# Kernel optimization log

Measured on AMD Instinct MI355X. Metric: run time of the kernel, lower is better.

## Reference

```python
import jax, jax.numpy as jnp
import numpy as np

B, T, N = 32, 64, 36
VD, H, S = 2048, 512, 300


def setup_inputs() -> dict:
    key = jax.random.key(0)
    ks = jax.random.split(key, 24)
    sc = 0.02
    d = {
        "visual": jax.random.normal(ks[0], (B, T, VD), jnp.float32),
        "objects": jax.random.normal(ks[1], (B, N, H), jnp.float32),
        # linear_layer
        "lin_W": jax.random.normal(ks[2], (H, VD), jnp.float32) * sc,
        "lin_b": jnp.zeros((H,), jnp.float32),
        # W, U projections
        "W_W": jax.random.normal(ks[3], (H, H), jnp.float32) * sc,
        "W_b": jnp.zeros((H,), jnp.float32),
        "U_W": jax.random.normal(ks[4], (H, H), jnp.float32) * sc,
        "U_b": jnp.zeros((H,), jnp.float32),
        # additive attention bias (torch.ones init)
        "b_attn": jnp.ones((H,), jnp.float32),
        # scoring vector w: Linear(H, 1)
        "w_W": jax.random.normal(ks[5], (1, H), jnp.float32) * sc,
        "w_b": jnp.zeros((1,), jnp.float32),
        # BiLSTM: input 2H, hidden H//2 per direction; gate order i,f,g,o
        "Wih_f": jax.random.normal(ks[6], (4 * (H // 2), 2 * H), jnp.float32) * sc,
        "Whh_f": jax.random.normal(ks[7], (4 * (H // 2), H // 2), jnp.float32) * sc,
        "bih_f": jnp.zeros((4 * (H // 2),), jnp.float32),
        "bhh_f": jnp.zeros((4 * (H // 2),), jnp.float32),
        "Wih_b": jax.random.normal(ks[8], (4 * (H // 2), 2 * H), jnp.float32) * sc,
        "Whh_b": jax.random.normal(ks[9], (4 * (H // 2), H // 2), jnp.float32) * sc,
        "bih_b": jnp.zeros((4 * (H // 2),), jnp.float32),
        "bhh_b": jnp.zeros((4 * (H // 2),), jnp.float32),
        # fc_layer
        "fc_W": jax.random.normal(ks[10], (S, H), jnp.float32) * sc,
        "fc_b": jnp.zeros((S,), jnp.float32),
    }
    return d


def _lstm(x, Wih, Whh, b):
    """Unidirectional LSTM over time. x: [B, T, D] -> [B, T, Hc]."""
    bsz = x.shape[0]
    Hc = Whh.shape[1]

    def step(carry, xt):
        h, c = carry
        g = xt @ Wih.T + h @ Whh.T + b          # [B, 4Hc]
        i, f, gg, o = jnp.split(g, 4, axis=-1)  # torch gate order i,f,g,o
        c = jax.nn.sigmoid(f) * c + jax.nn.sigmoid(i) * jnp.tanh(gg)
        h = jax.nn.sigmoid(o) * jnp.tanh(c)
        return (h, c), h

    h0 = jnp.zeros((bsz, Hc), x.dtype)
    _, hs = jax.lax.scan(step, (h0, h0), jnp.swapaxes(x, 0, 1))
    return jnp.swapaxes(hs, 0, 1)


def reference(visual, objects, lin_W, lin_b, W_W, W_b, U_W, U_b, b_attn,
              w_W, w_b, Wih_f, Whh_f, bih_f, bhh_f, Wih_b, Whh_b, bih_b,
              bhh_b, fc_W, fc_b):
    f3d = visual @ lin_W.T + lin_b                 # [B, T, H]
    Wf = f3d @ W_W.T + W_b                         # [B, T, H]
    Uo = objects @ U_W.T + U_b                     # [B, N, H]
    # broadcast additive attention: [B, T, N, H]
    attn_feat = Wf[:, :, None, :] + Uo[:, None, :, :] + b_attn
    scores = jnp.tanh(attn_feat) @ w_W.T + w_b     # [B, T, N, 1]
    attn_w = jax.nn.softmax(scores, axis=-2)       # softmax over objects N
    attn_obj = (attn_w * attn_feat).sum(axis=-2)   # [B, T, H]
    feats = jnp.concatenate([f3d, attn_obj], axis=-1)  # [B, T, 2H]
    out_f = _lstm(feats, Wih_f, Whh_f, bih_f + bhh_f)
    out_b = _lstm(feats[:, ::-1, :], Wih_b, Whh_b, bih_b + bhh_b)[:, ::-1, :]
    output = jnp.concatenate([out_f, out_b], axis=-1)  # [B, T, H]
    action = jnp.max(output, axis=1)                   # [B, H]
    action_semantics = action @ fc_W.T + fc_b          # [B, S]
    return output, action_semantics
```

## Files before the change

kernel.cpp:

```cpp
#include <hip/hip_runtime.h>
#include <hip/hip_bf16.h>
#include <type_traits>


typedef __hip_bfloat16 bf16;
typedef unsigned int uint32;
typedef __attribute__((ext_vector_type(8))) short s8v;
typedef __attribute__((ext_vector_type(4))) float f4v;
typedef __attribute__((ext_vector_type(4))) int   i32x4;

__device__ inline f4v mfma16(s8v a, s8v b, f4v c) {
    return __builtin_amdgcn_mfma_f32_16x16x32_bf16(a, b, c, 0, 0, 0);
}
__device__ inline float sigf(float x) {
    return __builtin_amdgcn_rcpf(1.f + __expf(-x));
}
__device__ inline float tanh_(float x) {
    return 1.f - 2.f * __builtin_amdgcn_rcpf(1.f + __expf(2.f * x));
}
__device__ inline void gload_lds16(const bf16* g, bf16* l) {
    __builtin_amdgcn_global_load_lds(
        (const __attribute__((address_space(1))) void*)g,
        (__attribute__((address_space(3))) void*)l, 16, 0, 0);
}

struct CvtJobs {
    const float* src[9];
    bf16*        dst[9];
    int          start[10];
};

__global__ __launch_bounds__(256) void cvt_kernel(CvtJobs jobs) {
    int blk = blockIdx.x;
    int j = 0;
#pragma unroll
    for (int i = 1; i < 9; ++i) if (blk >= jobs.start[i]) j = i;
    int off = (blk - jobs.start[j]) * 1024 + threadIdx.x * 4;
    float4 v = *(const float4*)(jobs.src[j] + off);
    union { bf16 h[4]; uint2 u; } p;
    p.h[0] = __float2bfloat16(v.x);
    p.h[1] = __float2bfloat16(v.y);
    p.h[2] = __float2bfloat16(v.z);
    p.h[3] = __float2bfloat16(v.w);
    *(uint2*)(jobs.dst[j] + off) = p.u;
}

template <typename CT>
__global__ __launch_bounds__(256) void gemm_tile(
    const bf16* __restrict__ A, int lda,
    const bf16* __restrict__ W,
    const float* __restrict__ b1, const float* __restrict__ b2,
    CT* __restrict__ C, int ldc,
    int K, int tiles_n, int permuteTB)
{
    __shared__ bf16 As[128 * 64];
    __shared__ bf16 Bs[128 * 64];

    int tid = threadIdx.x;
    int w = tid >> 6, lane = tid & 63;
    int lo = lane & 15, hi = lane >> 4;
    int mt = blockIdx.x / tiles_n, nt = blockIdx.x % tiles_n;
    int wm = w >> 1, wn = w & 1;

    const bf16* Ab = A + (size_t)(mt * 128) * lda;
    const bf16* Wb = W + (size_t)(nt * 128) * K;

    f4v acc[4][4];
#pragma unroll
    for (int m = 0; m < 4; ++m)
#pragma unroll
        for (int n = 0; n < 4; ++n) acc[m][n] = (f4v){0.f, 0.f, 0.f, 0.f};

    int wbase = tid & 192;

    for (int k0 = 0; k0 < K; k0 += 64) {
#pragma unroll
        for (int i = 0; i < 4; ++i) {
            int ci = i * 256 + tid;
            int row = ci >> 3, c = ci & 7;
            int gc = c ^ (row & 7);
            gload_lds16(Ab + (size_t)row * lda + k0 + gc * 8,
                        As + (i * 256 + wbase) * 8);
            gload_lds16(Wb + (size_t)row * K + k0 + gc * 8,
                        Bs + (i * 256 + wbase) * 8);
        }
        __syncthreads();

#pragma unroll
        for (int kt = 0; kt < 2; ++kt) {
            s8v a[4], b[4];
            int sw = ((kt * 4 + hi) ^ (lo & 7)) * 8;
#pragma unroll
            for (int m = 0; m < 4; ++m)
                a[m] = *(const s8v*)(As + (wm * 64 + m * 16 + lo) * 64 + sw);
#pragma unroll
            for (int n = 0; n < 4; ++n)
                b[n] = *(const s8v*)(Bs + (wn * 64 + n * 16 + lo) * 64 + sw);
#pragma unroll
            for (int m = 0; m < 4; ++m)
#pragma unroll
                for (int n = 0; n < 4; ++n)
                    acc[m][n] = mfma16(a[m], b[n], acc[m][n]);
        }
        __syncthreads();
    }

#pragma unroll
    for (int n = 0; n < 4; ++n) {
        int cc = nt * 128 + wn * 64 + n * 16 + lo;
        float bv = (b1 ? b1[cc] : 0.f) + (b2 ? b2[cc] : 0.f);
#pragma unroll
        for (int m = 0; m < 4; ++m) {
            int rbase = mt * 128 + wm * 64 + m * 16 + hi * 4;
#pragma unroll
            for (int i = 0; i < 4; ++i) {
                int r = rbase + i;
                int rr = permuteTB ? ((r & 63) * 32 + (r >> 6)) : r;
                float v = acc[m][n][i] + bv;
                if constexpr (std::is_same<CT, float>::value)
                    C[(size_t)rr * ldc + cc] = v;
                else
                    C[(size_t)rr * ldc + cc] = __float2bfloat16(v);
            }
        }
    }
}

__global__ __launch_bounds__(256) void attn_kernel(
    const float* __restrict__ Wf,
    const float* __restrict__ Uo,
    const float* __restrict__ wW,
    const float* __restrict__ wB,
    bf16* __restrict__ feats)
{
    int bt = blockIdx.x, b = bt >> 6;
    int wv = threadIdx.x >> 6, lane = threadIdx.x & 63;
    __shared__ float s_aw[36];

    float wfr[8], wr[8];
    const float* wfrow = Wf + (size_t)bt * 512 + lane * 8;
#pragma unroll
    for (int i = 0; i < 8; ++i) {
        wfr[i] = wfrow[i];
        wr[i]  = wW[lane * 8 + i];
    }
    float wbv = wB[0];

    for (int n = wv; n < 36; n += 4) {
        const float* uo = Uo + ((size_t)b * 36 + n) * 512 + lane * 8;
        float s = 0.f;
#pragma unroll
        for (int i = 0; i < 8; ++i) s += wr[i] * tanh_(wfr[i] + uo[i]);
#pragma unroll
        for (int off = 32; off; off >>= 1) s += __shfl_xor(s, off);
        if (lane == 0) s_aw[n] = s + wbv;
    }
    __syncthreads();
    if (threadIdx.x == 0) {
        float mx = -1e30f;
#pragma unroll
        for (int n = 0; n < 36; ++n) mx = fmaxf(mx, s_aw[n]);
        float e[36], sum = 0.f;
#pragma unroll
        for (int n = 0; n < 36; ++n) { e[n] = __expf(s_aw[n] - mx); sum += e[n]; }
        float r = __builtin_amdgcn_rcpf(sum);
#pragma unroll
        for (int n = 0; n < 36; ++n) s_aw[n] = e[n] * r;
    }
    __syncthreads();

    int h0 = threadIdx.x * 2;
    const float* wf2 = Wf + (size_t)bt * 512 + h0;
    float a0 = wf2[0], a1 = wf2[1];
    for (int n = 0; n < 36; ++n) {
        float awn = s_aw[n];
        const float* uo = Uo + ((size_t)b * 36 + n) * 512 + h0;
        a0 += awn * uo[0];
        a1 += awn * uo[1];
    }
    feats[(size_t)bt * 1024 + 512 + h0]     = __float2bfloat16(a0);
    feats[(size_t)bt * 1024 + 512 + h0 + 1] = __float2bfloat16(a1);
}

__device__ inline void poll4(const int* p, int need) {
    for (;;) {
        i32x4 f;
        asm volatile("global_load_dwordx4 %0, %1, off sc1\n\t"
                     "s_waitcnt vmcnt(0)"
                     : "=v"(f) : "v"(p) : "memory");
        if (f[0] >= need && f[1] >= need && f[2] >= need && f[3] >= need)
            break;
    }
}

__device__ inline void load_h16(const uint32* pF, const uint32* pB, s8v* aF) {
    asm volatile(
        "global_load_dwordx4 %0, %16, off sc1\n\t"
        "global_load_dwordx4 %1, %16, off offset:64 sc1\n\t"
        "global_load_dwordx4 %2, %16, off offset:128 sc1\n\t"
        "global_load_dwordx4 %3, %16, off offset:192 sc1\n\t"
        "global_load_dwordx4 %4, %16, off offset:256 sc1\n\t"
        "global_load_dwordx4 %5, %16, off offset:320 sc1\n\t"
        "global_load_dwordx4 %6, %16, off offset:384 sc1\n\t"
        "global_load_dwordx4 %7, %16, off offset:448 sc1\n\t"
        "global_load_dwordx4 %8, %17, off sc1\n\t"
        "global_load_dwordx4 %9, %17, off offset:64 sc1\n\t"
        "global_load_dwordx4 %10, %17, off offset:128 sc1\n\t"
        "global_load_dwordx4 %11, %17, off offset:192 sc1\n\t"
        "global_load_dwordx4 %12, %17, off offset:256 sc1\n\t"
        "global_load_dwordx4 %13, %17, off offset:320 sc1\n\t"
        "global_load_dwordx4 %14, %17, off offset:384 sc1\n\t"
        "global_load_dwordx4 %15, %17, off offset:448 sc1\n\t"
        "s_waitcnt vmcnt(0)"
        : "=v"(aF[0]), "=v"(aF[1]), "=v"(aF[2]), "=v"(aF[3]),
          "=v"(aF[4]), "=v"(aF[5]), "=v"(aF[6]), "=v"(aF[7]),
          "=v"(aF[8]), "=v"(aF[9]), "=v"(aF[10]), "=v"(aF[11]),
          "=v"(aF[12]), "=v"(aF[13]), "=v"(aF[14]), "=v"(aF[15])
        : "v"(pF), "v"(pB)
        : "memory");
}

__global__ __launch_bounds__(256, 1) void lstm_kernel(
    const bf16* __restrict__ WhhF, const bf16* __restrict__ WhhB,
    const float* __restrict__ gatesF, const float* __restrict__ gatesB,
    uint32* __restrict__ hx,
    float* __restrict__ out,
    int* __restrict__ bar)
{
    int bi  = blockIdx.x;
    int g   = bi >> 2;
    int pid = bi & 3;
    int jb  = pid * 64;
    int wv = threadIdx.x >> 6, lane = threadIdx.x & 63;
    int lo = lane & 15, hi = lane >> 4;
    int j0 = jb + wv * 16;

    uint32* hxg  = hx + (size_t)g * 8192;
    int*    flags = bar + g * 16;

    s8v whh[2][4][8];
#pragma unroll
    for (int q = 0; q < 4; ++q)
#pragma unroll
        for (int kt = 0; kt < 8; ++kt) {
            whh[0][q][kt] = *(const s8v*)(WhhF + (size_t)(q * 256 + j0 + lo) * 256 + kt * 32 + hi * 8);
            whh[1][q][kt] = *(const s8v*)(WhhB + (size_t)(q * 256 + j0 + lo) * 256 + kt * 32 + hi * 8);
        }

    int jbw = jb >> 1;
    for (int x = threadIdx.x; x < 1024; x += 256) {
        int d = x >> 9, b = (x >> 5) & 15, jw = jbw + (x & 31);
        __hip_atomic_store(&hxg[d * 4096 + b * 128 + jw], 0u,
                           __ATOMIC_RELAXED, __HIP_MEMORY_SCOPE_AGENT);
    }
    __syncthreads();
    if (threadIdx.x == 0)
        __hip_atomic_store(&flags[pid], 1, __ATOMIC_RELAXED,
                           __HIP_MEMORY_SCOPE_AGENT);

    poll4(flags, 1);
    s8v aF[16];
    {
        const uint32* pF = hxg + lo * 128 + hi * 4;
        load_h16(pF, pF + 4096, aF);
    }

    float cstf[4] = {0.f,0.f,0.f,0.f}, cstb[4] = {0.f,0.f,0.f,0.f};

    for (int t = 0; t < 64; ++t) {
        int tpF = t, tpB = 63 - t;
        int slot = (t + 1) & 1;

        float gvf[4][4], gvb[4][4];
#pragma unroll
        for (int i = 0; i < 4; ++i) {
            int bg = g * 16 + hi * 4 + i;
#pragma unroll
            for (int q = 0; q < 4; ++q) {
                gvf[q][i] = gatesF[(size_t)tpF * 32768 + bg * 1024 + q * 256 + j0 + lo];
                gvb[q][i] = gatesB[(size_t)tpB * 32768 + bg * 1024 + q * 256 + j0 + lo];
            }
        }

        float hvf[4];
        {
            f4v acc[4];
#pragma unroll
            for (int q = 0; q < 4; ++q) acc[q] = (f4v){0.f,0.f,0.f,0.f};
#pragma unroll
            for (int kt = 0; kt < 8; ++kt)
#pragma unroll
                for (int q = 0; q < 4; ++q)
                    acc[q] = mfma16(aF[kt], whh[0][q][kt], acc[q]);
#pragma unroll
            for (int i = 0; i < 4; ++i) {
                float xi = acc[0][i] + gvf[0][i];
                float xf = acc[1][i] + gvf[1][i];
                float xg = acc[2][i] + gvf[2][i];
                float xo = acc[3][i] + gvf[3][i];
                float c = sigf(xf) * cstf[i] + sigf(xi) * tanh_(xg);
                cstf[i] = c;
                hvf[i] = sigf(xo) * tanh_(c);
            }
        }
        if (t < 63) {
            uint32* hw = hxg + slot * 2048;
#pragma unroll
            for (int i = 0; i < 4; ++i) {
                float o2 = __shfl_xor(hvf[i], 1);
                if (!(lane & 1)) {
                    uint32 pk = (uint32)__bfloat16_as_ushort(__float2bfloat16(hvf[i]))
                              | ((uint32)__bfloat16_as_ushort(__float2bfloat16(o2)) << 16);
                    __hip_atomic_store(&hw[(hi * 4 + i) * 128 + ((j0 + lo) >> 1)], pk,
                                       __ATOMIC_RELAXED, __HIP_MEMORY_SCOPE_AGENT);
                }
            }
        }

        float hvb[4];
        {
            f4v acc[4];
#pragma unroll
            for (int q = 0; q < 4; ++q) acc[q] = (f4v){0.f,0.f,0.f,0.f};
#pragma unroll
            for (int kt = 0; kt < 8; ++kt)
#pragma unroll
                for (int q = 0; q < 4; ++q)
                    acc[q] = mfma16(aF[8 + kt], whh[1][q][kt], acc[q]);
#pragma unroll
            for (int i = 0; i < 4; ++i) {
                float xi = acc[0][i] + gvb[0][i];
                float xf = acc[1][i] + gvb[1][i];
                float xg = acc[2][i] + gvb[2][i];
                float xo = acc[3][i] + gvb[3][i];
                float c = sigf(xf) * cstb[i] + sigf(xi) * tanh_(xg);
                cstb[i] = c;
                hvb[i] = sigf(xo) * tanh_(c);
            }
        }
        if (t < 63) {
            uint32* hw = hxg + 4096 + slot * 2048;
#pragma unroll
            for (int i = 0; i < 4; ++i) {
                float o2 = __shfl_xor(hvb[i], 1);
                if (!(lane & 1)) {
                    uint32 pk = (uint32)__bfloat16_as_ushort(__float2bfloat16(hvb[i]))
                              | ((uint32)__bfloat16_as_ushort(__float2bfloat16(o2)) << 16);
                    __hip_atomic_store(&hw[(hi * 4 + i) * 128 + ((j0 + lo) >> 1)], pk,
                                       __ATOMIC_RELAXED, __HIP_MEMORY_SCOPE_AGENT);
                }
            }
        }

#pragma unroll
        for (int i = 0; i < 4; ++i) {
            int bg = g * 16 + hi * 4 + i;
            out[((size_t)bg * 64 + tpF) * 512 + j0 + lo]       = hvf[i];
            out[((size_t)bg * 64 + tpB) * 512 + 256 + j0 + lo] = hvb[i];
        }

        if (t < 63) {
            __syncthreads();
            if (threadIdx.x == 0)
                __hip_atomic_store(&flags[pid], t + 2, __ATOMIC_RELAXED,
                                   __HIP_MEMORY_SCOPE_AGENT);
            poll4(flags, t + 2);
            const uint32* pF = hxg + slot * 2048 + lo * 128 + hi * 4;
            load_h16(pF, pF + 4096, aF);
        }
    }
}

__global__ __launch_bounds__(256) void final_kernel(
    const float* __restrict__ out,
    const float* __restrict__ fcW,
    const float* __restrict__ fcb,
    float* __restrict__ osem)
{
    int b = blockIdx.x, tid = threadIdx.x;
    __shared__ float act[512];
    for (int h = tid; h < 512; h += 256) {
        float m = -1e30f;
        const float* p = out + (size_t)b * 64 * 512 + h;
#pragma unroll 8
        for (int t = 0; t < 64; ++t) m = fmaxf(m, p[t * 512]);
        act[h] = m;
    }
    __syncthreads();
    int wv = tid >> 6, lane = tid & 63;
    for (int s = wv; s < 300; s += 4) {
        const float* wrow = fcW + (size_t)s * 512 + lane * 8;
        float a = 0.f;
#pragma unroll
        for (int i = 0; i < 8; ++i) a += act[lane * 8 + i] * wrow[i];
#pragma unroll
        for (int off = 32; off; off >>= 1) a += __shfl_xor(a, off);
        if (lane == 0) osem[b * 300 + s] = a + fcb[s];
    }
}

extern "C" void kernel_launch(void* const* d_in, const int* in_sizes, int n_in,
                              void* d_out, int out_size, void* d_ws, size_t ws_size,
                              hipStream_t stream)
{
    const float* visual  = (const float*)d_in[0];
    const float* objects = (const float*)d_in[1];
    const float* lin_W   = (const float*)d_in[2];
    const float* lin_b   = (const float*)d_in[3];
    const float* W_W     = (const float*)d_in[4];
    const float* W_b     = (const float*)d_in[5];
    const float* U_W     = (const float*)d_in[6];
    const float* U_b     = (const float*)d_in[7];
    const float* b_attn  = (const float*)d_in[8];
    const float* w_W     = (const float*)d_in[9];
    const float* w_b     = (const float*)d_in[10];
    const float* Wih_f   = (const float*)d_in[11];
    const float* Whh_f   = (const float*)d_in[12];
    const float* bih_f   = (const float*)d_in[13];
    const float* bhh_f   = (const float*)d_in[14];
    const float* Wih_b   = (const float*)d_in[15];
    const float* Whh_b   = (const float*)d_in[16];
    const float* bih_b   = (const float*)d_in[17];
    const float* bhh_b   = (const float*)d_in[18];
    const float* fc_W    = (const float*)d_in[19];
    const float* fc_b    = (const float*)d_in[20];

    char* ws = (char*)d_ws;
    size_t o = 0;
    bf16*   feats   = (bf16*)(ws + o);   o += (size_t)2048 * 1024 * 2;
    float*  Wf      = (float*)(ws + o);  o += (size_t)2048 * 512 * 4;
    float*  Uo      = (float*)(ws + o);  o += (size_t)1152 * 512 * 4;
    float*  gatesF  = (float*)(ws + o);  o += (size_t)2048 * 1024 * 4;
    float*  gatesB  = (float*)(ws + o);  o += (size_t)2048 * 1024 * 4;
    uint32* hx      = (uint32*)(ws + o); o += (size_t)2 * 8192 * 4;
    int*    bar     = (int*)(ws + o);    o += 256;
    bf16*  visual_b  = (bf16*)(ws + o); o += (size_t)4194304 * 2;
    bf16*  objects_b = (bf16*)(ws + o); o += (size_t)589824 * 2;
    bf16*  lin_Wb    = (bf16*)(ws + o); o += (size_t)1048576 * 2;
    bf16*  W_Wb      = (bf16*)(ws + o); o += (size_t)262144 * 2;
    bf16*  U_Wb      = (bf16*)(ws + o); o += (size_t)262144 * 2;
    bf16*  Wih_fb    = (bf16*)(ws + o); o += (size_t)1048576 * 2;
    bf16*  Whh_fb    = (bf16*)(ws + o); o += (size_t)262144 * 2;
    bf16*  Wih_bb    = (bf16*)(ws + o); o += (size_t)1048576 * 2;
    bf16*  Whh_bb    = (bf16*)(ws + o); o += (size_t)262144 * 2;

    CvtJobs cj;
    const float* srcs[9] = {visual, objects, lin_W, W_W, U_W, Wih_f, Whh_f, Wih_b, Whh_b};
    bf16* dsts[9] = {visual_b, objects_b, lin_Wb, W_Wb, U_Wb, Wih_fb, Whh_fb, Wih_bb, Whh_bb};
    int ns[9] = {4194304, 589824, 1048576, 262144, 262144, 1048576, 262144, 1048576, 262144};
    int acc_b = 0;
    for (int i = 0; i < 9; ++i) {
        cj.src[i] = srcs[i];
        cj.dst[i] = dsts[i];
        cj.start[i] = acc_b;
        acc_b += ns[i] / 1024;
    }
    cj.start[9] = acc_b;

    dim3 blk(256);
    cvt_kernel<<<acc_b, blk, 0, stream>>>(cj);

    gemm_tile<bf16><<<64, blk, 0, stream>>>(visual_b, 2048, lin_Wb, lin_b, nullptr,
                                            feats, 1024, 2048, 4, 0);
    gemm_tile<float><<<36, blk, 0, stream>>>(objects_b, 512, U_Wb, U_b, b_attn,
                                             Uo, 512, 512, 4, 0);
    gemm_tile<float><<<64, blk, 0, stream>>>(feats, 1024, W_Wb, W_b, nullptr,
                                             Wf, 512, 512, 4, 0);
    attn_kernel<<<2048, blk, 0, stream>>>(Wf, Uo, w_W, w_b, feats);
    gemm_tile<float><<<128, blk, 0, stream>>>(feats, 1024, Wih_fb, bih_f, bhh_f,
                                              gatesF, 1024, 1024, 8, 1);
    gemm_tile<float><<<128, blk, 0, stream>>>(feats, 1024, Wih_bb, bih_b, bhh_b,
                                              gatesB, 1024, 1024, 8, 1);
    lstm_kernel<<<8, blk, 0, stream>>>(Whh_fb, Whh_bb, gatesF, gatesB, hx,
                                       (float*)d_out, bar);
    final_kernel<<<32, blk, 0, stream>>>((float*)d_out, fc_W, fc_b,
                                         (float*)d_out + 1048576);
}
```

Measured before the change: 591.7 us.

## Replace cross-block LSTM barrier with per-block recurrence; merge GEMM launches, bf16 gates

The LSTM recurrence is restructured so that each 512-thread block owns one direction and 16 batch rows with all 256 hidden units. The whole Whh matrix is held in registers plus LDS, and h is exchanged through shared memory with __syncthreads. This replaces the old global-memory flag polling across 4 blocks per group. The input-gate GEMMs are merged into a single launch that writes bf16 gates, and the pre-GEMMs are fused into one launch with smaller 64-row tiles for more blocks. Softmax in the attention kernel now uses wave shuffles instead of a single thread. The trade-off is that only 4 blocks run the serial recurrence, each doing more MFMA work per step, and storing gates in bf16 loses precision.

New measurement: 782.6 us. 1.32x slower.

```diff
diff --git a/kernel.cpp b/kernel.cpp
--- a/kernel.cpp
+++ b/kernel.cpp
@@ -5,9 +5,9 @@
 
 typedef __hip_bfloat16 bf16;
 typedef unsigned int uint32;
+typedef unsigned short ushort_t;
 typedef __attribute__((ext_vector_type(8))) short s8v;
 typedef __attribute__((ext_vector_type(4))) float f4v;
-typedef __attribute__((ext_vector_type(4))) int   i32x4;
 
 __device__ inline f4v mfma16(s8v a, s8v b, f4v c) {
     return __builtin_amdgcn_mfma_f32_16x16x32_bf16(a, b, c, 0, 0, 0);
@@ -17,6 +17,12 @@
 }
 __device__ inline float tanh_(float x) {
     return 1.f - 2.f * __builtin_amdgcn_rcpf(1.f + __expf(2.f * x));
+}
+__device__ inline float bf2f(ushort_t u) {
+    union { uint32 i; float f; } p; p.i = (uint32)u << 16; return p.f;
+}
+__device__ inline ushort_t f2bf(float f) {
+    return __bfloat16_as_ushort(__float2bfloat16(f));
 }
 __device__ inline void gload_lds16(const bf16* g, bf16* l) {
     __builtin_amdgcn_global_load_lds(
@@ -45,29 +51,25 @@
     *(uint2*)(jobs.dst[j] + off) = p.u;
 }
 
-template <typename CT>
-__global__ __launch_bounds__(256) void gemm_tile(
+template <int MT>
+__device__ inline void gemm_body(
+    bf16* As, bf16* Bs,
     const bf16* __restrict__ A, int lda,
     const bf16* __restrict__ W,
     const float* __restrict__ b1, const float* __restrict__ b2,
-    CT* __restrict__ C, int ldc,
-    int K, int tiles_n, int permuteTB)
-{
-    __shared__ bf16 As[128 * 64];
-    __shared__ bf16 Bs[128 * 64];
-
+    void* C, int ldc, int K, int mt, int nt, int obf, int permuteTB)
+{
     int tid = threadIdx.x;
     int w = tid >> 6, lane = tid & 63;
     int lo = lane & 15, hi = lane >> 4;
-    int mt = blockIdx.x / tiles_n, nt = blockIdx.x % tiles_n;
     int wm = w >> 1, wn = w & 1;
 
-    const bf16* Ab = A + (size_t)(mt * 128) * lda;
+    const bf16* Ab = A + (size_t)(mt * (MT * 32)) * lda;
     const bf16* Wb = W + (size_t)(nt * 128) * K;
 
-    f4v acc[4][4];
-#pragma unroll
-    for (int m = 0; m < 4; ++m)
+    f4v acc[MT][4];
+#pragma unroll
+    for (int m = 0; m < MT; ++m)
 #pragma unroll
         for (int n = 0; n < 4; ++n) acc[m][n] = (f4v){0.f, 0.f, 0.f, 0.f};
 
@@ -75,12 +77,18 @@
 
     for (int k0 = 0; k0 < K; k0 += 64) {
 #pragma unroll
-        for (int i = 0; i < 4; ++i) {
+        for (int i = 0; i < MT; ++i) {
             int ci = i * 256 + tid;
             int row = ci >> 3, c = ci & 7;
             int gc = c ^ (row & 7);
             gload_lds16(Ab + (size_t)row * lda + k0 + gc * 8,
                         As + (i * 256 + wbase) * 8);
+        }
+#pragma unroll
+        for (int i = 0; i < 4; ++i) {
+            int ci = i * 256 + tid;
+            int row = ci >> 3, c = ci & 7;
+            int gc = c ^ (row & 7);
             gload_lds16(Wb + (size_t)row * K + k0 + gc * 8,
                         Bs + (i * 256 + wbase) * 8);
         }
@@ -88,16 +96,16 @@
 
 #pragma unroll
         for (int kt = 0; kt < 2; ++kt) {
-            s8v a[4], b[4];
+            s8v a[MT], b[4];
             int sw = ((kt * 4 + hi) ^ (lo & 7)) * 8;
 #pragma unroll
-            for (int m = 0; m < 4; ++m)
-                a[m] = *(const s8v*)(As + (wm * 64 + m * 16 + lo) * 64 + sw);
+            for (int m = 0; m < MT; ++m)
+                a[m] = *(const s8v*)(As + (wm * (MT * 16) + m * 16 + lo) * 64 + sw);
 #pragma unroll
             for (int n = 0; n < 4; ++n)
                 b[n] = *(const s8v*)(Bs + (wn * 64 + n * 16 + lo) * 64 + sw);
 #pragma unroll
-            for (int m = 0; m < 4; ++m)
+            for (int m = 0; m < MT; ++m)
 #pragma unroll
                 for (int n = 0; n < 4; ++n)
                     acc[m][n] = mfma16(a[m], b[n], acc[m][n]);
@@ -110,20 +118,61 @@
         int cc = nt * 128 + wn * 64 + n * 16 + lo;
         float bv = (b1 ? b1[cc] : 0.f) + (b2 ? b2[cc] : 0.f);
 #pragma unroll
-        for (int m = 0; m < 4; ++m) {
-            int rbase = mt * 128 + wm * 64 + m * 16 + hi * 4;
+        for (int m = 0; m < MT; ++m) {
+            int rbase = mt * (MT * 32) + wm * (MT * 16) + m * 16 + hi * 4;
 #pragma unroll
             for (int i = 0; i < 4; ++i) {
                 int r = rbase + i;
                 int rr = permuteTB ? ((r & 63) * 32 + (r >> 6)) : r;
                 float v = acc[m][n][i] + bv;
-                if constexpr (std::is_same<CT, float>::value)
-                    C[(size_t)rr * ldc + cc] = v;
-                else
-                    C[(size_t)rr * ldc + cc] = __float2bfloat16(v);
+                if (obf) ((bf16*)C)[(size_t)rr * ldc + cc] = __float2bfloat16(v);
+                else     ((float*)C)[(size_t)rr * ldc + cc] = v;
             }
         }
     }
+}
+
+__global__ __launch_bounds__(256) void gemm_pre(
+    const bf16* visual_b, const bf16* lin_Wb, const float* lin_b,
+    const bf16* objects_b, const bf16* U_Wb, const float* U_b,
+    const float* b_attn, bf16* feats, float* Uo)
+{
+    __shared__ bf16 As[64 * 64];
+    __shared__ bf16 Bs[128 * 64];
+    int blk = blockIdx.x;
+    if (blk < 128)
+        gemm_body<2>(As, Bs, visual_b, 2048, lin_Wb, lin_b, nullptr,
+                     feats, 1024, 2048, blk / 4, blk % 4, 1, 0);
+    else {
+        int bi = blk - 128;
+        gemm_body<2>(As, Bs, objects_b, 512, U_Wb, U_b, b_attn,
+                     Uo, 512, 512, bi / 4, bi % 4, 0, 0);
+    }
+}
+
+__global__ __launch_bounds__(256) void gemm_wf(
+    const bf16* feats, const bf16* W_Wb, const float* W_b, float* Wf)
+{
+    __shared__ bf16 As[64 * 64];
+    __shared__ bf16 Bs[128 * 64];
+    gemm_body<2>(As, Bs, feats, 1024, W_Wb, W_b, nullptr,
+                 Wf, 512, 512, blockIdx.x / 4, blockIdx.x % 4, 0, 0);
+}
+
+__global__ __launch_bounds__(256) void gemm_gates(
+    const bf16* feats, const bf16* Wih_fb, const bf16* Wih_bb,
+    const float* bih_f, const float* bhh_f,
+    const float* bih_b, const float* bhh_b, bf16* gatesFB)
+{
+    __shared__ bf16 As[128 * 64];
+    __shared__ bf16 Bs[128 * 64];
+    int sel = blockIdx.x >> 7;
+    int blk = blockIdx.x & 127;
+    gemm_body<4>(As, Bs, feats, 1024,
+                 sel ? Wih_bb : Wih_fb,
+                 sel ? bih_b : bih_f, sel ? bhh_b : bhh_f,
+                 gatesFB + (size_t)sel * 2097152, 1024, 1024,
+                 blk / 8, blk % 8, 1, 1);
 }
 
 __global__ __launch_bounds__(256) void attn_kernel(
@@ -156,16 +205,16 @@
         if (lane == 0) s_aw[n] = s + wbv;
     }
     __syncthreads();
-    if (threadIdx.x == 0) {
-        float mx = -1e30f;
-#pragma unroll
-        for (int n = 0; n < 36; ++n) mx = fmaxf(mx, s_aw[n]);
-        float e[36], sum = 0.f;
-#pragma unroll
-        for (int n = 0; n < 36; ++n) { e[n] = __expf(s_aw[n] - mx); sum += e[n]; }
-        float r = __builtin_amdgcn_rcpf(sum);
-#pragma unroll
-        for (int n = 0; n < 36; ++n) s_aw[n] = e[n] * r;
+    if (threadIdx.x < 64) {
+        float v = (lane < 36) ? s_aw[lane] : -1e30f;
+        float mx = v;
+#pragma unroll
+        for (int off = 32; off; off >>= 1) mx = fmaxf(mx, __shfl_xor(mx, off));
+        float e = (lane < 36) ? __expf(v - mx) : 0.f;
+        float sum = e;
+#pragma unroll
+        for (int off = 32; off; off >>= 1) sum += __shfl_xor(sum, off);
+        if (lane < 36) s_aw[lane] = e * __builtin_amdgcn_rcpf(sum);
     }
     __syncthreads();
 
@@ -182,192 +231,103 @@
     feats[(size_t)bt * 1024 + 512 + h0 + 1] = __float2bfloat16(a1);
 }
 
-__device__ inline void poll4(const int* p, int need) {
-    for (;;) {
-        i32x4 f;
-        asm volatile("global_load_dwordx4 %0, %1, off sc1\n\t"
-                     "s_waitcnt vmcnt(0)"
-                     : "=v"(f) : "v"(p) : "memory");
-        if (f[0] >= need && f[1] >= need && f[2] >= need && f[3] >= need)
-            break;
-    }
-}
-
-__device__ inline void load_h16(const uint32* pF, const uint32* pB, s8v* aF) {
-    asm volatile(
-        "global_load_dwordx4 %0, %16, off sc1\n\t"
-        "global_load_dwordx4 %1, %16, off offset:64 sc1\n\t"
-        "global_load_dwordx4 %2, %16, off offset:128 sc1\n\t"
-        "global_load_dwordx4 %3, %16, off offset:192 sc1\n\t"
-        "global_load_dwordx4 %4, %16, off offset:256 sc1\n\t"
-        "global_load_dwordx4 %5, %16, off offset:320 sc1\n\t"
-        "global_load_dwordx4 %6, %16, off offset:384 sc1\n\t"
-        "global_load_dwordx4 %7, %16, off offset:448 sc1\n\t"
-        "global_load_dwordx4 %8, %17, off sc1\n\t"
-        "global_load_dwordx4 %9, %17, off offset:64 sc1\n\t"
-        "global_load_dwordx4 %10, %17, off offset:128 sc1\n\t"
-        "global_load_dwordx4 %11, %17, off offset:192 sc1\n\t"
-        "global_load_dwordx4 %12, %17, off offset:256 sc1\n\t"
-        "global_load_dwordx4 %13, %17, off offset:320 sc1\n\t"
-        "global_load_dwordx4 %14, %17, off offset:384 sc1\n\t"
-        "global_load_dwordx4 %15, %17, off offset:448 sc1\n\t"
-        "s_waitcnt vmcnt(0)"
-        : "=v"(aF[0]), "=v"(aF[1]), "=v"(aF[2]), "=v"(aF[3]),
-          "=v"(aF[4]), "=v"(aF[5]), "=v"(aF[6]), "=v"(aF[7]),
-          "=v"(aF[8]), "=v"(aF[9]), "=v"(aF[10]), "=v"(aF[11]),
-          "=v"(aF[12]), "=v"(aF[13]), "=v"(aF[14]), "=v"(aF[15])
-        : "v"(pF), "v"(pB)
-        : "memory");
-}
-
-__global__ __launch_bounds__(256, 1) void lstm_kernel(
+__global__ __launch_bounds__(512, 2) void lstm_kernel(
     const bf16* __restrict__ WhhF, const bf16* __restrict__ WhhB,
-    const float* __restrict__ gatesF, const float* __restrict__ gatesB,
-    uint32* __restrict__ hx,
-    float* __restrict__ out,
-    int* __restrict__ bar)
-{
-    int bi  = blockIdx.x;
-    int g   = bi >> 2;
-    int pid = bi & 3;
-    int jb  = pid * 64;
-    int wv = threadIdx.x >> 6, lane = threadIdx.x & 63;
+    const bf16* __restrict__ gates,
+    float* __restrict__ out)
+{
+    __shared__ ushort_t sh_h[16 * 256];
+    __shared__ ushort_t sh_whh[8 * 18 * 512];
+
+    int dir = blockIdx.x >> 1;
+    int g   = blockIdx.x & 1;
+    int w    = threadIdx.x >> 6;
+    int lane = threadIdx.x & 63;
     int lo = lane & 15, hi = lane >> 4;
-    int j0 = jb + wv * 16;
-
-    uint32* hxg  = hx + (size_t)g * 8192;
-    int*    flags = bar + g * 16;
-
-    s8v whh[2][4][8];
-#pragma unroll
-    for (int q = 0; q < 4; ++q)
+
+    const bf16* Whh = dir ? WhhB : WhhF;
+    const ushort_t* gb = (const ushort_t*)gates + (size_t)dir * 2097152;
+
+    s8v whhR[46];
+#pragma unroll
+    for (int q2h = 0; q2h < 8; ++q2h) {
+        int jf = (q2h >> 1) * 16 + w * 2 + (q2h & 1);
+        const bf16* wp = Whh + (size_t)(jf * 16 + lo) * 256 + hi * 8;
 #pragma unroll
         for (int kt = 0; kt < 8; ++kt) {
-            whh[0][q][kt] = *(const s8v*)(WhhF + (size_t)(q * 256 + j0 + lo) * 256 + kt * 32 + hi * 8);
-            whh[1][q][kt] = *(const s8v*)(WhhB + (size_t)(q * 256 + j0 + lo) * 256 + kt * 32 + hi * 8);
-        }
-
-    int jbw = jb >> 1;
-    for (int x = threadIdx.x; x < 1024; x += 256) {
-        int d = x >> 9, b = (x >> 5) & 15, jw = jbw + (x & 31);
-        __hip_atomic_store(&hxg[d * 4096 + b * 128 + jw], 0u,
-                           __ATOMIC_RELAXED, __HIP_MEMORY_SCOPE_AGENT);
-    }
+            int f = q2h * 8 + kt;
+            if (f < 46) whhR[f] = *(const s8v*)(wp + kt * 32);
+            else gload_lds16(wp + kt * 32,
+                             (bf16*)&sh_whh[(w * 18 + (f - 46)) * 512]);
+        }
+    }
+
+    for (int x = threadIdx.x; x < 4096; x += 512) sh_h[x] = 0;
+
+    float cst[2][4] = {{0.f,0.f,0.f,0.f},{0.f,0.f,0.f,0.f}};
     __syncthreads();
-    if (threadIdx.x == 0)
-        __hip_atomic_store(&flags[pid], 1, __ATOMIC_RELAXED,
-                           __HIP_MEMORY_SCOPE_AGENT);
-
-    poll4(flags, 1);
-    s8v aF[16];
-    {
-        const uint32* pF = hxg + lo * 128 + hi * 4;
-        load_h16(pF, pF + 4096, aF);
-    }
-
-    float cstf[4] = {0.f,0.f,0.f,0.f}, cstb[4] = {0.f,0.f,0.f,0.f};
 
     for (int t = 0; t < 64; ++t) {
-        int tpF = t, tpB = 63 - t;
-        int slot = (t + 1) & 1;
-
-        float gvf[4][4], gvb[4][4];
-#pragma unroll
-        for (int i = 0; i < 4; ++i) {
-            int bg = g * 16 + hi * 4 + i;
-#pragma unroll
-            for (int q = 0; q < 4; ++q) {
-                gvf[q][i] = gatesF[(size_t)tpF * 32768 + bg * 1024 + q * 256 + j0 + lo];
-                gvb[q][i] = gatesB[(size_t)tpB * 32768 + bg * 1024 + q * 256 + j0 + lo];
-            }
-        }
-
-        float hvf[4];
+        int tp = dir ? (63 - t) : t;
+
+        f4v acc[8];
         {
-            f4v acc[4];
-#pragma unroll
-            for (int q = 0; q < 4; ++q) acc[q] = (f4v){0.f,0.f,0.f,0.f};
-#pragma unroll
-            for (int kt = 0; kt < 8; ++kt)
-#pragma unroll
-                for (int q = 0; q < 4; ++q)
-                    acc[q] = mfma16(aF[kt], whh[0][q][kt], acc[q]);
-#pragma unroll
-            for (int i = 0; i < 4; ++i) {
-                float xi = acc[0][i] + gvf[0][i];
-                float xf = acc[1][i] + gvf[1][i];
-                float xg = acc[2][i] + gvf[2][i];
-                float xo = acc[3][i] + gvf[3][i];
-                float c = sigf(xf) * cstf[i] + sigf(xi) * tanh_(xg);
-                cstf[i] = c;
-                hvf[i] = sigf(xo) * tanh_(c);
-            }
-        }
-        if (t < 63) {
-            uint32* hw = hxg + slot * 2048;
-#pragma unroll
-            for (int i = 0; i < 4; ++i) {
-                float o2 = __shfl_xor(hvf[i], 1);
-                if (!(lane & 1)) {
-                    uint32 pk = (uint32)__bfloat16_as_ushort(__float2bfloat16(hvf[i]))
-                              | ((uint32)__bfloat16_as_ushort(__float2bfloat16(o2)) << 16);
-                    __hip_atomic_store(&hw[(hi * 4 + i) * 128 + ((j0 + lo) >> 1)], pk,
-                                       __ATOMIC_RELAXED, __HIP_MEMORY_SCOPE_AGENT);
+            const ushort_t* gt = gb + (size_t)tp * 32768 + (g * 16) * 1024;
+#pragma unroll
+            for (int q = 0; q < 4; ++q)
+#pragma unroll
+                for (int half = 0; half < 2; ++half) {
+                    int col = q * 256 + w * 32 + half * 16 + lo;
+#pragma unroll
+                    for (int i = 0; i < 4; ++i)
+                        acc[q * 2 + half][i] = bf2f(gt[(hi * 4 + i) * 1024 + col]);
+                }
+        }
+
+#pragma unroll
+        for (int kt = 0; kt < 8; ++kt) {
+            s8v a = *(const s8v*)&sh_h[lo * 256 + (((kt * 4 + hi) ^ (lo & 7)) * 8)];
+#pragma unroll
+            for (int q2h = 0; q2h < 8; ++q2h) {
+                int f = q2h * 8 + kt;
+                if (f < 46) {
+                    acc[q2h] = mfma16(a, whhR[f], acc[q2h]);
+                } else {
+                    s8v bb = *(const s8v*)&sh_whh[(w * 18 + (f - 46)) * 512 + lane * 8];
+                    acc[q2h] = mfma16(a, bb, acc[q2h]);
                 }
             }
         }
 
-        float hvb[4];
-        {
-            f4v acc[4];
-#pragma unroll
-            for (int q = 0; q < 4; ++q) acc[q] = (f4v){0.f,0.f,0.f,0.f};
-#pragma unroll
-            for (int kt = 0; kt < 8; ++kt)
-#pragma unroll
-                for (int q = 0; q < 4; ++q)
-                    acc[q] = mfma16(aF[8 + kt], whh[1][q][kt], acc[q]);
+        float hv[2][4];
+#pragma unroll
+        for (int half = 0; half < 2; ++half)
 #pragma unroll
             for (int i = 0; i < 4; ++i) {
-                float xi = acc[0][i] + gvb[0][i];
-                float xf = acc[1][i] + gvb[1][i];
-                float xg = acc[2][i] + gvb[2][i];
-                float xo = acc[3][i] + gvb[3][i];
-                float c = sigf(xf) * cstb[i] + sigf(xi) * tanh_(xg);
-                cstb[i] = c;
-                hvb[i] = sigf(xo) * tanh_(c);
+                float xi = acc[0 + half][i];
+                float xf = acc[2 + half][i];
+                float xg = acc[4 + half][i];
+                float xo = acc[6 + half][i];
+                float c = sigf(xf) * cst[half][i] + sigf(xi) * tanh_(xg);
+                cst[half][i] = c;
+                hv[half][i] = sigf(xo) * tanh_(c);
             }
-        }
-        if (t < 63) {
-            uint32* hw = hxg + 4096 + slot * 2048;
+
+        __syncthreads();
+
+#pragma unroll
+        for (int half = 0; half < 2; ++half)
 #pragma unroll
             for (int i = 0; i < 4; ++i) {
-                float o2 = __shfl_xor(hvb[i], 1);
-                if (!(lane & 1)) {
-                    uint32 pk = (uint32)__bfloat16_as_ushort(__float2bfloat16(hvb[i]))
-                              | ((uint32)__bfloat16_as_ushort(__float2bfloat16(o2)) << 16);
-                    __hip_atomic_store(&hw[(hi * 4 + i) * 128 + ((j0 + lo) >> 1)], pk,
-                                       __ATOMIC_RELAXED, __HIP_MEMORY_SCOPE_AGENT);
-                }
+                int b = hi * 4 + i;
+                int c = w * 32 + half * 16 + lo;
+                int slot = (c >> 3) ^ (b & 7);
+                sh_h[b * 256 + slot * 8 + (lo & 7)] = f2bf(hv[half][i]);
+                out[((size_t)(g * 16 + b) * 64 + tp) * 512 + dir * 256 + c] =
+                    hv[half][i];
             }
-        }
-
-#pragma unroll
-        for (int i = 0; i < 4; ++i) {
-            int bg = g * 16 + hi * 4 + i;
-            out[((size_t)bg * 64 + tpF) * 512 + j0 + lo]       = hvf[i];
-            out[((size_t)bg * 64 + tpB) * 512 + 256 + j0 + lo] = hvb[i];
-        }
-
-        if (t < 63) {
-            __syncthreads();
-            if (threadIdx.x == 0)
-                __hip_atomic_store(&flags[pid], t + 2, __ATOMIC_RELAXED,
-                                   __HIP_MEMORY_SCOPE_AGENT);
-            poll4(flags, t + 2);
-            const uint32* pF = hxg + slot * 2048 + lo * 128 + hi * 4;
-            load_h16(pF, pF + 4096, aF);
-        }
+
+        __syncthreads();
     }
 }
 
@@ -430,10 +390,7 @@
     bf16*   feats   = (bf16*)(ws + o);   o += (size_t)2048 * 1024 * 2;
     float*  Wf      = (float*)(ws + o);  o += (size_t)2048 * 512 * 4;
     float*  Uo      = (float*)(ws + o);  o += (size_t)1152 * 512 * 4;
-    float*  gatesF  = (float*)(ws + o);  o += (size_t)2048 * 1024 * 4;
-    float*  gatesB  = (float*)(ws + o);  o += (size_t)2048 * 1024 * 4;
-    uint32* hx      = (uint32*)(ws + o); o += (size_t)2 * 8192 * 4;
-    int*    bar     = (int*)(ws + o);    o += 256;
+    bf16*   gatesFB = (bf16*)(ws + o);   o += (size_t)2 * 2097152 * 2;
     bf16*  visual_b  = (bf16*)(ws + o); o += (size_t)4194304 * 2;
     bf16*  objects_b = (bf16*)(ws + o); o += (size_t)589824 * 2;
     bf16*  lin_Wb    = (bf16*)(ws + o); o += (size_t)1048576 * 2;
@@ -460,19 +417,14 @@
     dim3 blk(256);
     cvt_kernel<<<acc_b, blk, 0, stream>>>(cj);
 
-    gemm_tile<bf16><<<64, blk, 0, stream>>>(visual_b, 2048, lin_Wb, lin_b, nullptr,
-                                            feats, 1024, 2048, 4, 0);
-    gemm_tile<float><<<36, blk, 0, stream>>>(objects_b, 512, U_Wb, U_b, b_attn,
-                                             Uo, 512, 512, 4, 0);
-    gemm_tile<float><<<64, blk, 0, stream>>>(feats, 1024, W_Wb, W_b, nullptr,
-                                             Wf, 512, 512, 4, 0);
+    gemm_pre<<<200, blk, 0, stream>>>(visual_b, lin_Wb, lin_b,
+                                      objects_b, U_Wb, U_b, b_attn, feats, Uo);
+    gemm_wf<<<128, blk, 0, stream>>>(feats, W_Wb, W_b, Wf);
     attn_kernel<<<2048, blk, 0, stream>>>(Wf, Uo, w_W, w_b, feats);
-    gemm_tile<float><<<128, blk, 0, stream>>>(feats, 1024, Wih_fb, bih_f, bhh_f,
-                                              gatesF, 1024, 1024, 8, 1);
-    gemm_tile<float><<<128, blk, 0, stream>>>(feats, 1024, Wih_bb, bih_b, bhh_b,
-                                              gatesB, 1024, 1024, 8, 1);
-    lstm_kernel<<<8, blk, 0, stream>>>(Whh_fb, Whh_bb, gatesF, gatesB, hx,
-                                       (float*)d_out, bar);
+    gemm_gates<<<256, blk, 0, stream>>>(feats, Wih_fb, Wih_bb,
+                                        bih_f, bhh_f, bih_b, bhh_b, gatesFB);
+    lstm_kernel<<<4, dim3(512), 0, stream>>>(Whh_fb, Whh_bb, gatesFB,
+                                             (float*)d_out);
     final_kernel<<<32, blk, 0, stream>>>((float*)d_out, fc_W, fc_b,
                                          (float*)d_out + 1048576);
 }
```
